# Kernel optimization log

Hardware: AMD Instinct MI355X
Metric: run time of the kernel (lower is better)

The kernel has to match this reference:

```python
import jax, jax.numpy as jnp
import numpy as np

IN_FEATURES = 1024
OUT_FEATURES = 1024
GRID_SIZE = 5
SPLINE_ORDER = 3
GRID_RANGE = (-1.0, 1.0)


def make_grid():
    h = (GRID_RANGE[1] - GRID_RANGE[0]) / GRID_SIZE
    knots = jnp.arange(-SPLINE_ORDER, GRID_SIZE + SPLINE_ORDER + 1, dtype=jnp.float32) * h + GRID_RANGE[0]
    return jnp.broadcast_to(knots, (IN_FEATURES, knots.shape[0]))  # (in, 12)


def b_splines(x, knots, p):
    # x: (B, in); knots: (in, nk). Cox-de Boor recursion, degree p.
    xs = x[:, :, None]                                   # (B, in, 1)
    bases = ((xs >= knots[None, :, :-1]) & (xs < knots[None, :, 1:])).astype(x.dtype)
    for k in range(1, p + 1):
        den1 = knots[:, k:-1] - knots[:, :-(k + 1)]
        den1 = jnp.where(den1 == 0, jnp.float32(1e-8), den1)
        den2 = knots[:, k + 1:] - knots[:, 1:-k]
        den2 = jnp.where(den2 == 0, jnp.float32(1e-8), den2)
        term1 = (xs - knots[None, :, :-(k + 1)]) / den1[None] * bases[:, :, :-1]
        term2 = (knots[None, :, k + 1:] - xs) / den2[None] * bases[:, :, 1:]
        bases = term1 + term2
    return bases  # (B, in, grid_size + p)


def setup_inputs() -> dict:
    key = jax.random.key(0)
    k1, k2, k3, k4 = jax.random.split(key, 4)
    K = GRID_SIZE + SPLINE_ORDER
    x = jax.random.normal(k1, (4096, IN_FEATURES), dtype=jnp.float32)
    base_weight = jax.random.normal(k2, (OUT_FEATURES, IN_FEATURES), dtype=jnp.float32) * (1.0 / np.sqrt(IN_FEATURES))
    spline_weight = jax.random.normal(k3, (OUT_FEATURES, IN_FEATURES, K), dtype=jnp.float32) * 0.02
    spline_scaler = jax.random.normal(k4, (OUT_FEATURES, IN_FEATURES), dtype=jnp.float32) * (1.0 / np.sqrt(IN_FEATURES))
    grid = make_grid()
    return {"x": x, "base_weight": base_weight, "spline_weight": spline_weight,
            "spline_scaler": spline_scaler, "grid": grid}


def reference(x, base_weight, spline_weight, spline_scaler, grid):
    base_out = jax.nn.silu(x) @ base_weight.T                      # (B, out)
    bases = b_splines(x, grid, SPLINE_ORDER)                       # (B, in, K)
    scaled_sw = spline_weight * spline_scaler[:, :, None]          # (out, in, K)
    spline_out = jnp.einsum('bik,oik->bo', bases, scaled_sw)       # (B, out)
    return base_out + spline_out
```

## Files before the change

kernel.cpp:

```cpp
#include <hip/hip_runtime.h>
#include <hip/hip_bf16.h>
#include <cstdint>
#include <cstddef>

#define AS1 __attribute__((address_space(1)))
#define AS3 __attribute__((address_space(3)))

typedef __bf16 bf16;
typedef __bf16 bf16x8 __attribute__((ext_vector_type(8)));
typedef float f32x4 __attribute__((ext_vector_type(4)));

static constexpr int M_ROWS = 4096;
static constexpr int N_COLS = 1024;
static constexpr int IN_F   = 1024;
static constexpr int K2     = IN_F * 9;
static constexpr int BK     = 32;
static constexpr int KT_CNT = K2 / BK;

static constexpr int GBK = 64;
static constexpr int GKT = K2 / GBK;


__device__ __forceinline__ void bases8(float x, float w8[8]) {
  float mf = x * 2.5f + 5.5f;
  int   m  = (int)floorf(mf);
  float u  = mf - (float)m;
  float u2 = u * u, u3 = u2 * u;
  float omu = 1.0f - u;
  const float s = 1.0f / 6.0f;
  float p0 = u3 * s;
  float p1 = (-3.f*u3 + 3.f*u2 + 3.f*u + 1.f) * s;
  float p2 = (3.f*u3 - 6.f*u2 + 4.f) * s;
  float p3 = omu * omu * omu * s;
  bool in = (m >= 0) && (m < 11);
#pragma unroll
  for (int j = 0; j < 8; ++j) {
    float v = 0.0f;
    v = (j == m)     ? p0 : v;
    v = (j == m - 1) ? p1 : v;
    v = (j == m - 2) ? p2 : v;
    v = (j == m - 3) ? p3 : v;
    w8[j] = in ? v : 0.0f;
  }
}

__device__ __forceinline__ void expand_body(const float* __restrict__ x,
                                            bf16* __restrict__ A, int gid, int r0) {
  int b = gid >> 10;
  int i = gid & 1023;
  float xv = x[(size_t)r0 * IN_F + (size_t)gid];
  A[(size_t)b * K2 + i] = (bf16)(xv / (1.0f + __expf(-xv)));
  float w8[8];
  bases8(xv, w8);
  bf16x8 outv;
#pragma unroll
  for (int j = 0; j < 8; ++j) outv[j] = (bf16)w8[j];
  *(bf16x8*)(A + (size_t)b * K2 + IN_F + (size_t)i * 8) = outv;
}

__device__ __forceinline__ void makebt_body(const float* __restrict__ bw,
                                            const float* __restrict__ sw,
                                            const float* __restrict__ sc,
                                            bf16* __restrict__ BT, int gid) {
  int o = gid >> 10;
  int i = gid & 1023;
  BT[(size_t)o * K2 + i] = (bf16)bw[gid];
  float scale = sc[gid];
  const float4* swp = (const float4*)(sw + (size_t)gid * 8);
  float4 a = swp[0], b4 = swp[1];
  float wv[8] = {a.x, a.y, a.z, a.w, b4.x, b4.y, b4.z, b4.w};
  bf16x8 r;
#pragma unroll
  for (int j = 0; j < 8; ++j) r[j] = (bf16)(wv[j] * scale);
  *(bf16x8*)(BT + (size_t)o * K2 + IN_F + (size_t)i * 8) = r;
}

__global__ void prep(const float* __restrict__ x, const float* __restrict__ bw,
                     const float* __restrict__ sw, const float* __restrict__ sc,
                     bf16* __restrict__ A, bf16* __restrict__ BT) {
  int bid = blockIdx.x;
  if (bid < (M_ROWS * IN_F) / 256) {
    expand_body(x, A, bid * 256 + threadIdx.x, 0);
  } else {
    makebt_body(bw, sw, sc, BT, (bid - (M_ROWS * IN_F) / 256) * 256 + threadIdx.x);
  }
}

__global__ void expand_a(const float* __restrict__ x, bf16* __restrict__ A, int r0) {
  expand_body(x, A, blockIdx.x * blockDim.x + threadIdx.x, r0);
}
__global__ void make_bt(const float* __restrict__ bw, const float* __restrict__ sw,
                        const float* __restrict__ sc, bf16* __restrict__ BT) {
  makebt_body(bw, sw, sc, BT, blockIdx.x * blockDim.x + threadIdx.x);
}

__global__ __launch_bounds__(512, 2) void gemm256_8p(
    const bf16* __restrict__ A, const bf16* __restrict__ BT,
    float* __restrict__ P, int kt_seg) {
  __shared__ bf16 As[2][256 * GBK];
  __shared__ bf16 Bs[2][256 * GBK];

  const int tid  = threadIdx.x;
  const int lane = tid & 63;
  const int w    = tid >> 6;

  const int b     = blockIdx.x;
  const int mtile = b & 15;
  const int np    = (b >> 4) & 3;
  const int seg   = b >> 6;
  const int row0  = mtile * 256;
  const int col0  = np * 256;
  const int kt0   = seg * kt_seg;
  float* __restrict__ dst = P + (size_t)seg * M_ROWS * N_COLS;

  const int srow = lane >> 3;
  const int sch  = ((lane & 7) ^ srow) * 8;

  const int r  = lane & 15;
  const int q  = lane >> 4;
  const int wm = (w >> 2) * 128;
  const int wn = (w & 3) * 64;
  const int kc0 = ((0 + q) ^ (r & 7)) * 8;
  const int kc1 = ((4 + q) ^ (r & 7)) * 8;

  const bf16* aB = A  + (size_t)row0 * K2;
  const bf16* bB = BT + (size_t)col0 * K2;

  f32x4 acc[8][4];
#pragma unroll
  for (int mt = 0; mt < 8; ++mt)
#pragma unroll
    for (int nt = 0; nt < 4; ++nt)
      acc[mt][nt] = f32x4{0.f, 0.f, 0.f, 0.f};

  auto stageA = [&](int sbuf, int h, int kt) {
#pragma unroll
    for (int t8 = 0; t8 < 2; ++t8) {
      const int rg = h * 128 + w * 16 + t8 * 8;
      const bf16* ga = aB + (size_t)(rg + srow) * K2 + kt * GBK + sch;
      __builtin_amdgcn_global_load_lds((const AS1 void*)ga,
                                       (AS3 void*)&As[sbuf][rg * GBK], 16, 0, 0);
    }
  };
  auto stageB = [&](int sbuf, int h, int kt) {
#pragma unroll
    for (int t8 = 0; t8 < 2; ++t8) {
      const int rg = h * 128 + w * 16 + t8 * 8;
      const bf16* gb = bB + (size_t)(rg + srow) * K2 + kt * GBK + sch;
      __builtin_amdgcn_global_load_lds((const AS1 void*)gb,
                                       (AS3 void*)&Bs[sbuf][rg * GBK], 16, 0, 0);
    }
  };

  stageA(0, 0, kt0); stageA(0, 1, kt0);
  stageB(0, 0, kt0); stageB(0, 1, kt0);
  if (kt_seg > 1) stageA(1, 0, kt0 + 1);
  if (kt_seg > 1) asm volatile("s_waitcnt vmcnt(2)" ::: "memory");
  else            asm volatile("s_waitcnt vmcnt(0)" ::: "memory");
  __builtin_amdgcn_s_barrier();

  bf16x8 af[4][2], bfr[4][2];

  for (int t = 0; t < kt_seg; ++t) {
    const int buf = t & 1, nbuf = buf ^ 1;
    const bf16* as = As[buf];
    const bf16* bs = Bs[buf];
    const bool sN = (t + 1 < kt_seg);

#pragma unroll
    for (int j = 0; j < 4; ++j) {
      const bf16* ar = &as[(wm + j * 16 + r) * GBK];
      af[j][0] = *(const bf16x8*)&ar[kc0];
      af[j][1] = *(const bf16x8*)&ar[kc1];
    }
#pragma unroll
    for (int j = 0; j < 2; ++j) {
      const bf16* br = &bs[(wn + j * 16 + r) * GBK];
      bfr[j][0] = *(const bf16x8*)&br[kc0];
      bfr[j][1] = *(const bf16x8*)&br[kc1];
    }
    if (sN) stageA(nbuf, 1, kt0 + t + 1);
    asm volatile("s_waitcnt lgkmcnt(8)" ::: "memory");
    __builtin_amdgcn_s_barrier();
    asm volatile("s_waitcnt lgkmcnt(0)" ::: "memory");
    __builtin_amdgcn_sched_barrier(0);
    __builtin_amdgcn_s_setprio(1);
#pragma unroll
    for (int j = 0; j < 4; ++j)
#pragma unroll
      for (int n = 0; n < 2; ++n) {
        acc[j][n] = __builtin_amdgcn_mfma_f32_16x16x32_bf16(af[j][0], bfr[n][0], acc[j][n], 0, 0, 0);
        acc[j][n] = __builtin_amdgcn_mfma_f32_16x16x32_bf16(af[j][1], bfr[n][1], acc[j][n], 0, 0, 0);
      }
    __builtin_amdgcn_s_setprio(0);
    __builtin_amdgcn_s_barrier();

#pragma unroll
    for (int j = 0; j < 2; ++j) {
      const bf16* br = &bs[(wn + (2 + j) * 16 + r) * GBK];
      bfr[2 + j][0] = *(const bf16x8*)&br[kc0];
      bfr[2 + j][1] = *(const bf16x8*)&br[kc1];
    }
    if (sN) stageB(nbuf, 0, kt0 + t + 1);
    __builtin_amdgcn_s_barrier();
    asm volatile("s_waitcnt lgkmcnt(0)" ::: "memory");
    __builtin_amdgcn_sched_barrier(0);
    __builtin_amdgcn_s_setprio(1);
#pragma unroll
    for (int j = 0; j < 4; ++j)
#pragma unroll
      for (int n = 0; n < 2; ++n) {
        acc[j][2 + n] = __builtin_amdgcn_mfma_f32_16x16x32_bf16(af[j][0], bfr[2 + n][0], acc[j][2 + n], 0, 0, 0);
        acc[j][2 + n] = __builtin_amdgcn_mfma_f32_16x16x32_bf16(af[j][1], bfr[2 + n][1], acc[j][2 + n], 0, 0, 0);
      }
    __builtin_amdgcn_s_setprio(0);
    __builtin_amdgcn_s_barrier();

#pragma unroll
    for (int j = 0; j < 4; ++j) {
      const bf16* ar = &as[(wm + (4 + j) * 16 + r) * GBK];
      af[j][0] = *(const bf16x8*)&ar[kc0];
      af[j][1] = *(const bf16x8*)&ar[kc1];
    }
    if (sN) stageB(nbuf, 1, kt0 + t + 1);
    __builtin_amdgcn_s_barrier();
    asm volatile("s_waitcnt lgkmcnt(0)" ::: "memory");
    __builtin_amdgcn_sched_barrier(0);
    __builtin_amdgcn_s_setprio(1);
#pragma unroll
    for (int j = 0; j < 4; ++j)
#pragma unroll
      for (int n = 0; n < 2; ++n) {
        acc[4 + j][n] = __builtin_amdgcn_mfma_f32_16x16x32_bf16(af[j][0], bfr[n][0], acc[4 + j][n], 0, 0, 0);
        acc[4 + j][n] = __builtin_amdgcn_mfma_f32_16x16x32_bf16(af[j][1], bfr[n][1], acc[4 + j][n], 0, 0, 0);
      }
    __builtin_amdgcn_s_setprio(0);
    __builtin_amdgcn_s_barrier();

    if (t + 2 < kt_seg) stageA(buf, 0, kt0 + t + 2);
    if (sN) {
      if (t + 2 < kt_seg) asm volatile("s_waitcnt vmcnt(2)" ::: "memory");
      else                asm volatile("s_waitcnt vmcnt(0)" ::: "memory");
    }
    __builtin_amdgcn_s_barrier();
    __builtin_amdgcn_s_setprio(1);
#pragma unroll
    for (int j = 0; j < 4; ++j)
#pragma unroll
      for (int n = 0; n < 2; ++n) {
        acc[4 + j][2 + n] = __builtin_amdgcn_mfma_f32_16x16x32_bf16(af[j][0], bfr[2 + n][0], acc[4 + j][2 + n], 0, 0, 0);
        acc[4 + j][2 + n] = __builtin_amdgcn_mfma_f32_16x16x32_bf16(af[j][1], bfr[2 + n][1], acc[4 + j][2 + n], 0, 0, 0);
      }
    __builtin_amdgcn_s_setprio(0);
    __builtin_amdgcn_s_barrier();
  }

#pragma unroll
  for (int mt = 0; mt < 8; ++mt)
#pragma unroll
    for (int nt = 0; nt < 4; ++nt)
#pragma unroll
      for (int k = 0; k < 4; ++k) {
        int row = row0 + wm + mt * 16 + q * 4 + k;
        int col = col0 + wn + nt * 16 + r;
        dst[(size_t)row * N_COLS + col] = acc[mt][nt][k];
      }
}

__global__ __launch_bounds__(256, 2) void gemm_fused(
    const bf16* __restrict__ A, const bf16* __restrict__ BT,
    float* __restrict__ d0, float* __restrict__ d1,
    int r0, int mt_cnt, int kt_seg) {
  __shared__ bf16 As[2][128 * GBK];
  __shared__ bf16 Bs[2][128 * GBK];

  const int tid  = threadIdx.x;
  const int lane = tid & 63;
  const int w    = tid >> 6;

  const int bps = mt_cnt * 8;
  int b   = blockIdx.x;
  const int seg = b / bps;
  b -= seg * bps;
  const int row0 = (b % mt_cnt) * 128;
  const int col0 = (b / mt_cnt) * 128;
  float* __restrict__ dst = seg ? d1 : d0;
  const int kt0 = seg * kt_seg;

  const int srow = lane >> 3;
  const int sch  = ((lane & 7) ^ srow) * 8;
  const int r  = lane & 15;
  const int q  = lane >> 4;
  const int wm = (w >> 1) * 64;
  const int wn = (w & 1) * 64;
  const int kc0 = ((0 + q) ^ (r & 7)) * 8;
  const int kc1 = ((4 + q) ^ (r & 7)) * 8;

  const bf16* aB = A  + (size_t)row0 * K2;
  const bf16* bB = BT + (size_t)col0 * K2;

  f32x4 acc[4][4];
#pragma unroll
  for (int mt = 0; mt < 4; ++mt)
#pragma unroll
    for (int nt = 0; nt < 4; ++nt)
      acc[mt][nt] = f32x4{0.f, 0.f, 0.f, 0.f};

  auto stage = [&](int sbuf, int kt) {
#pragma unroll
    for (int t = 0; t < 4; ++t) {
      const int rg = w * 32 + t * 8;
      const bf16* ga = aB + (size_t)(rg + srow) * K2 + kt * GBK + sch;
      __builtin_amdgcn_global_load_lds((const AS1 void*)ga,
                                       (AS3 void*)&As[sbuf][rg * GBK], 16, 0, 0);
      const bf16* gb = bB + (size_t)(rg + srow) * K2 + kt * GBK + sch;
      __builtin_amdgcn_global_load_lds((const AS1 void*)gb,
                                       (AS3 void*)&Bs[sbuf][rg * GBK], 16, 0, 0);
    }
  };

  stage(0, kt0);
  int buf = 0;
  for (int i = 0; i < kt_seg; ++i) {
    if (i + 1 < kt_seg) {
      stage(buf ^ 1, kt0 + i + 1);
      asm volatile("s_waitcnt vmcnt(8)" ::: "memory");
    } else {
      asm volatile("s_waitcnt vmcnt(0)" ::: "memory");
    }
    __builtin_amdgcn_s_barrier();
    __builtin_amdgcn_sched_barrier(0);

    const bf16* as = As[buf];
    const bf16* bs = Bs[buf];

#pragma unroll
    for (int kk = 0; kk < 2; ++kk) {
      const int kc = kk ? kc1 : kc0;
      bf16x8 af[4], bfr[4];
#pragma unroll
      for (int mt = 0; mt < 4; ++mt)
        af[mt] = *(const bf16x8*)&as[(wm + mt * 16 + r) * GBK + kc];
#pragma unroll
      for (int nt = 0; nt < 4; ++nt)
        bfr[nt] = *(const bf16x8*)&bs[(wn + nt * 16 + r) * GBK + kc];
#pragma unroll
      for (int mt = 0; mt < 4; ++mt)
#pragma unroll
        for (int nt = 0; nt < 4; ++nt)
          acc[mt][nt] = __builtin_amdgcn_mfma_f32_16x16x32_bf16(
              af[mt], bfr[nt], acc[mt][nt], 0, 0, 0);
    }
    __builtin_amdgcn_s_barrier();
    buf ^= 1;
  }

#pragma unroll
  for (int mt = 0; mt < 4; ++mt)
#pragma unroll
    for (int nt = 0; nt < 4; ++nt)
#pragma unroll
      for (int k = 0; k < 4; ++k) {
        int row = r0 + row0 + wm + mt * 16 + q * 4 + k;
        int col = col0 + wn + nt * 16 + r;
        dst[(size_t)row * N_COLS + col] = acc[mt][nt][k];
      }
}

__global__ void reduce_addN(const float* __restrict__ P,
                            float* __restrict__ out, int segs) {
  size_t i = (size_t)blockIdx.x * blockDim.x + threadIdx.x;
  const f32x4* p = (const f32x4*)P;
  const size_t plane = (size_t)M_ROWS * N_COLS / 4;
  f32x4 a = p[i];
  for (int s = 1; s < segs; ++s) a += p[(size_t)s * plane + i];
  ((f32x4*)out)[i] = a;
}

__global__ __launch_bounds__(256) void kan_fused_fallback(
    const float* __restrict__ x, const float* __restrict__ bw,
    const float* __restrict__ sw, const float* __restrict__ sc,
    float* __restrict__ out) {
  __shared__ bf16 As[64 * BK];
  __shared__ bf16 Bs[128 * BK];
  const int tid  = threadIdx.x;
  const int lane = tid & 63;
  const int w    = tid >> 6;
  const int col0 = blockIdx.x * 128;
  const int row0 = blockIdx.y * 64;
  const int srow = tid >> 2, sq = tid & 3;
  const int r = lane & 15, q = lane >> 4, wn = w * 32;

  f32x4 acc[4][2];
#pragma unroll
  for (int mt = 0; mt < 4; ++mt)
#pragma unroll
    for (int nt = 0; nt < 2; ++nt) acc[mt][nt] = f32x4{0,0,0,0};

  for (int kt = 0; kt < KT_CNT; ++kt) {
    if (kt < 32) {
      const int cc = sq * 8;
      const float4* xp = (const float4*)(x + (size_t)(row0+srow)*IN_F + kt*BK + cc);
      float4 a = xp[0], b4 = xp[1];
      float xv[8] = {a.x,a.y,a.z,a.w,b4.x,b4.y,b4.z,b4.w};
      bf16x8 av;
#pragma unroll
      for (int j = 0; j < 8; ++j) av[j] = (bf16)(xv[j] / (1.0f + __expf(-xv[j])));
      *(bf16x8*)&As[srow * BK + cc] = av;
#pragma unroll
      for (int h = 0; h < 2; ++h) {
        const float4* bp = (const float4*)(bw + (size_t)(col0+h*64+srow)*IN_F + kt*BK + cc);
        float4 c0 = bp[0], c1 = bp[1];
        float bv[8] = {c0.x,c0.y,c0.z,c0.w,c1.x,c1.y,c1.z,c1.w};
        bf16x8 bb;
#pragma unroll
        for (int j = 0; j < 8; ++j) bb[j] = (bf16)bv[j];
        *(bf16x8*)&Bs[(h*64+srow)*BK + cc] = bb;
      }
    } else {
      const int i = (kt - 32) * 4 + sq;
      float xv = x[(size_t)(row0+srow)*IN_F + i];
      float w8[8]; bases8(xv, w8);
      bf16x8 av;
#pragma unroll
      for (int j = 0; j < 8; ++j) av[j] = (bf16)w8[j];
      *(bf16x8*)&As[srow * BK + sq * 8] = av;
#pragma unroll
      for (int h = 0; h < 2; ++h) {
        const int o = col0 + h*64 + srow;
        float s1 = sc[(size_t)o*IN_F + i];
        const float4* sp = (const float4*)(sw + ((size_t)o*IN_F + i)*8);
        float4 c0 = sp[0], c1 = sp[1];
        float wv[8] = {c0.x,c0.y,c0.z,c0.w,c1.x,c1.y,c1.z,c1.w};
        bf16x8 bb;
#pragma unroll
        for (int j = 0; j < 8; ++j) bb[j] = (bf16)(wv[j]*s1);
        *(bf16x8*)&Bs[(h*64+srow)*BK + sq*8] = bb;
      }
    }
    __syncthreads();
    bf16x8 af[4], bfr[2];
#pragma unroll
    for (int mt = 0; mt < 4; ++mt)
      af[mt] = *(const bf16x8*)&As[(mt*16+r)*BK + q*8];
#pragma unroll
    for (int nt = 0; nt < 2; ++nt)
      bfr[nt] = *(const bf16x8*)&Bs[(wn+nt*16+r)*BK + q*8];
#pragma unroll
    for (int mt = 0; mt < 4; ++mt)
#pragma unroll
      for (int nt = 0; nt < 2; ++nt)
        acc[mt][nt] = __builtin_amdgcn_mfma_f32_16x16x32_bf16(af[mt], bfr[nt], acc[mt][nt], 0,0,0);
    __syncthreads();
  }
#pragma unroll
  for (int mt = 0; mt < 4; ++mt)
#pragma unroll
    for (int nt = 0; nt < 2; ++nt)
#pragma unroll
      for (int k = 0; k < 4; ++k)
        out[(size_t)(row0+mt*16+q*4+k)*N_COLS + col0+wn+nt*16+r] = acc[mt][nt][k];
}

extern "C" void kernel_launch(void* const* d_in, const int* in_sizes, int n_in,
                              void* d_out, int out_size, void* d_ws, size_t ws_size,
                              hipStream_t stream) {
  const float* x    = (const float*)d_in[0];
  const float* bw   = (const float*)d_in[1];
  const float* sw   = (const float*)d_in[2];
  const float* sc   = (const float*)d_in[3];
  float* out = (float*)d_out;

  const size_t BT_BYTES  = (size_t)N_COLS * K2 * sizeof(bf16);
  const size_t ROW_BYTES = (size_t)K2 * sizeof(bf16);
  const size_t A_BYTES   = (size_t)M_ROWS * ROW_BYTES;
  const size_t OUT_BYTES = (size_t)M_ROWS * N_COLS * sizeof(float);

  int S = 0;
  for (int c = 4; c >= 2; --c)
    if (GKT % c == 0 && BT_BYTES + A_BYTES + (size_t)c * OUT_BYTES <= ws_size) {
      S = c; break;
    }

  if (S >= 2) {
    bf16*  BT    = (bf16*)d_ws;
    bf16*  Aslab = BT + (size_t)N_COLS * K2;
    float* P     = (float*)((char*)d_ws + BT_BYTES + A_BYTES);
    prep<<<(M_ROWS * IN_F) / 256 + (N_COLS * IN_F) / 256, 256, 0, stream>>>(
        x, bw, sw, sc, Aslab, BT);
    gemm256_8p<<<S * 64, 512, 0, stream>>>(Aslab, BT, P, GKT / S);
    reduce_addN<<<(M_ROWS * N_COLS) / (4 * 256), 256, 0, stream>>>(P, out, S);
  } else {
    int SL = 0;
    for (int cand = 4096; cand >= 128; cand >>= 1)
      if (BT_BYTES + (size_t)cand * ROW_BYTES <= ws_size) { SL = cand; break; }
    if (SL) {
      bf16* BT    = (bf16*)d_ws;
      bf16* Aslab = BT + (size_t)N_COLS * K2;
      make_bt<<<(N_COLS * IN_F) / 256, 256, 0, stream>>>(bw, sw, sc, BT);
      for (int r0 = 0; r0 < M_ROWS; r0 += SL) {
        expand_a<<<(SL * IN_F) / 256, 256, 0, stream>>>(x, Aslab, r0);
        gemm_fused<<<(SL / 128) * (N_COLS / 128), 256, 0, stream>>>(
            Aslab, BT, out, out, r0, SL / 128, GKT);
      }
    } else {
      kan_fused_fallback<<<dim3(N_COLS / 128, M_ROWS / 64), 256, 0, stream>>>(
          x, bw, sw, sc, out);
    }
  }
  (void)in_sizes; (void)n_in; (void)out_size;
}
```

Baseline: 201.2 us.

## Software-pipeline LDS fragment reads across K-tiles with reordered MFMA quadrants

Restructures the main GEMM loop so each quadrant's LDS fragment reads are issued one MFMA phase ahead. The first A and B fragments of the next K-tile are prefetched during the last MFMA phase of the current tile, and the loop is unrolled by two to ping-pong the B fragment registers. This cuts the number of barriers per tile and hides LDS latency behind MFMA work, at the cost of more live registers. The host now requires an even number of K-tiles per split.

```diff
diff --git a/kernel.cpp b/kernel.cpp
--- a/kernel.cpp
+++ b/kernel.cpp
@@ -94,7 +94,7 @@
   makebt_body(bw, sw, sc, BT, blockIdx.x * blockDim.x + threadIdx.x);
 }
 
-__global__ __launch_bounds__(512, 2) void gemm256_8p(
+__global__ __launch_bounds__(512, 2) void gemm256_pl(
     const bf16* __restrict__ A, const bf16* __restrict__ BT,
     float* __restrict__ P, int kt_seg) {
   __shared__ bf16 As[2][256 * GBK];
@@ -133,6 +133,8 @@
     for (int nt = 0; nt < 4; ++nt)
       acc[mt][nt] = f32x4{0.f, 0.f, 0.f, 0.f};
 
+  bf16x8 af03[4][2], af47[4][2], bf23[2][2], bf01A[2][2], bf01B[2][2];
+
   auto stageA = [&](int sbuf, int h, int kt) {
 #pragma unroll
     for (int t8 = 0; t8 < 2; ++t8) {
@@ -152,107 +154,125 @@
     }
   };
 
-  stageA(0, 0, kt0); stageA(0, 1, kt0);
-  stageB(0, 0, kt0); stageB(0, 1, kt0);
-  if (kt_seg > 1) stageA(1, 0, kt0 + 1);
-  if (kt_seg > 1) asm volatile("s_waitcnt vmcnt(2)" ::: "memory");
-  else            asm volatile("s_waitcnt vmcnt(0)" ::: "memory");
-  __builtin_amdgcn_s_barrier();
-
-  bf16x8 af[4][2], bfr[4][2];
-
-  for (int t = 0; t < kt_seg; ++t) {
-    const int buf = t & 1, nbuf = buf ^ 1;
-    const bf16* as = As[buf];
-    const bf16* bs = Bs[buf];
+  auto readA03 = [&](const bf16* src) {
+#pragma unroll
+    for (int j = 0; j < 4; ++j) {
+      const bf16* ar = &src[(wm + j * 16 + r) * GBK];
+      af03[j][0] = *(const bf16x8*)&ar[kc0];
+      af03[j][1] = *(const bf16x8*)&ar[kc1];
+    }
+  };
+  auto readA47 = [&](const bf16* src) {
+#pragma unroll
+    for (int j = 0; j < 4; ++j) {
+      const bf16* ar = &src[(wm + (4 + j) * 16 + r) * GBK];
+      af47[j][0] = *(const bf16x8*)&ar[kc0];
+      af47[j][1] = *(const bf16x8*)&ar[kc1];
+    }
+  };
+  auto readB23 = [&](const bf16* src) {
+#pragma unroll
+    for (int j = 0; j < 2; ++j) {
+      const bf16* br = &src[(wn + (2 + j) * 16 + r) * GBK];
+      bf23[j][0] = *(const bf16x8*)&br[kc0];
+      bf23[j][1] = *(const bf16x8*)&br[kc1];
+    }
+  };
+  auto readB01 = [&](bf16x8 (&dstf)[2][2], const bf16* src) {
+#pragma unroll
+    for (int j = 0; j < 2; ++j) {
+      const bf16* br = &src[(wn + j * 16 + r) * GBK];
+      dstf[j][0] = *(const bf16x8*)&br[kc0];
+      dstf[j][1] = *(const bf16x8*)&br[kc1];
+    }
+  };
+
+  auto tile_body = [&](int t, int nb, const bf16* as, const bf16* bs,
+                       const bf16* nas, const bf16* nbs,
+                       bf16x8 (&bfc)[2][2], bf16x8 (&bfn)[2][2]) {
     const bool sN = (t + 1 < kt_seg);
 
-#pragma unroll
-    for (int j = 0; j < 4; ++j) {
-      const bf16* ar = &as[(wm + j * 16 + r) * GBK];
-      af[j][0] = *(const bf16x8*)&ar[kc0];
-      af[j][1] = *(const bf16x8*)&ar[kc1];
-    }
-#pragma unroll
-    for (int j = 0; j < 2; ++j) {
-      const bf16* br = &bs[(wn + j * 16 + r) * GBK];
-      bfr[j][0] = *(const bf16x8*)&br[kc0];
-      bfr[j][1] = *(const bf16x8*)&br[kc1];
-    }
-    if (sN) stageA(nbuf, 1, kt0 + t + 1);
+    readB23(bs);
+    if (sN) stageA(nb, 1, kt0 + t + 1);
+    asm volatile("s_waitcnt lgkmcnt(4)" ::: "memory");
+    __builtin_amdgcn_sched_barrier(0);
+    __builtin_amdgcn_s_barrier();
+    __builtin_amdgcn_s_setprio(1);
+#pragma unroll
+    for (int j = 0; j < 4; ++j)
+#pragma unroll
+      for (int n = 0; n < 2; ++n) {
+        acc[j][n] = __builtin_amdgcn_mfma_f32_16x16x32_bf16(af03[j][0], bfc[n][0], acc[j][n], 0, 0, 0);
+        acc[j][n] = __builtin_amdgcn_mfma_f32_16x16x32_bf16(af03[j][1], bfc[n][1], acc[j][n], 0, 0, 0);
+      }
+    __builtin_amdgcn_s_setprio(0);
+
+    readA47(as);
+    if (sN) stageB(nb, 0, kt0 + t + 1);
     asm volatile("s_waitcnt lgkmcnt(8)" ::: "memory");
+    __builtin_amdgcn_sched_barrier(0);
     __builtin_amdgcn_s_barrier();
+    __builtin_amdgcn_s_setprio(1);
+#pragma unroll
+    for (int j = 0; j < 4; ++j)
+#pragma unroll
+      for (int n = 0; n < 2; ++n) {
+        acc[j][2 + n] = __builtin_amdgcn_mfma_f32_16x16x32_bf16(af03[j][0], bf23[n][0], acc[j][2 + n], 0, 0, 0);
+        acc[j][2 + n] = __builtin_amdgcn_mfma_f32_16x16x32_bf16(af03[j][1], bf23[n][1], acc[j][2 + n], 0, 0, 0);
+      }
+    __builtin_amdgcn_s_setprio(0);
+
+    if (sN) stageB(nb, 1, kt0 + t + 1);
     asm volatile("s_waitcnt lgkmcnt(0)" ::: "memory");
     __builtin_amdgcn_sched_barrier(0);
+    __builtin_amdgcn_s_barrier();
     __builtin_amdgcn_s_setprio(1);
 #pragma unroll
     for (int j = 0; j < 4; ++j)
 #pragma unroll
       for (int n = 0; n < 2; ++n) {
-        acc[j][n] = __builtin_amdgcn_mfma_f32_16x16x32_bf16(af[j][0], bfr[n][0], acc[j][n], 0, 0, 0);
-        acc[j][n] = __builtin_amdgcn_mfma_f32_16x16x32_bf16(af[j][1], bfr[n][1], acc[j][n], 0, 0, 0);
+        acc[4 + j][2 + n] = __builtin_amdgcn_mfma_f32_16x16x32_bf16(af47[j][0], bf23[n][0], acc[4 + j][2 + n], 0, 0, 0);
+        acc[4 + j][2 + n] = __builtin_amdgcn_mfma_f32_16x16x32_bf16(af47[j][1], bf23[n][1], acc[4 + j][2 + n], 0, 0, 0);
       }
     __builtin_amdgcn_s_setprio(0);
-    __builtin_amdgcn_s_barrier();
-
-#pragma unroll
-    for (int j = 0; j < 2; ++j) {
-      const bf16* br = &bs[(wn + (2 + j) * 16 + r) * GBK];
-      bfr[2 + j][0] = *(const bf16x8*)&br[kc0];
-      bfr[2 + j][1] = *(const bf16x8*)&br[kc1];
-    }
-    if (sN) stageB(nbuf, 0, kt0 + t + 1);
-    __builtin_amdgcn_s_barrier();
-    asm volatile("s_waitcnt lgkmcnt(0)" ::: "memory");
-    __builtin_amdgcn_sched_barrier(0);
-    __builtin_amdgcn_s_setprio(1);
-#pragma unroll
-    for (int j = 0; j < 4; ++j)
-#pragma unroll
-      for (int n = 0; n < 2; ++n) {
-        acc[j][2 + n] = __builtin_amdgcn_mfma_f32_16x16x32_bf16(af[j][0], bfr[2 + n][0], acc[j][2 + n], 0, 0, 0);
-        acc[j][2 + n] = __builtin_amdgcn_mfma_f32_16x16x32_bf16(af[j][1], bfr[2 + n][1], acc[j][2 + n], 0, 0, 0);
-      }
-    __builtin_amdgcn_s_setprio(0);
-    __builtin_amdgcn_s_barrier();
-
-#pragma unroll
-    for (int j = 0; j < 4; ++j) {
-      const bf16* ar = &as[(wm + (4 + j) * 16 + r) * GBK];
-      af[j][0] = *(const bf16x8*)&ar[kc0];
-      af[j][1] = *(const bf16x8*)&ar[kc1];
-    }
-    if (sN) stageB(nbuf, 1, kt0 + t + 1);
-    __builtin_amdgcn_s_barrier();
-    asm volatile("s_waitcnt lgkmcnt(0)" ::: "memory");
-    __builtin_amdgcn_sched_barrier(0);
-    __builtin_amdgcn_s_setprio(1);
-#pragma unroll
-    for (int j = 0; j < 4; ++j)
-#pragma unroll
-      for (int n = 0; n < 2; ++n) {
-        acc[4 + j][n] = __builtin_amdgcn_mfma_f32_16x16x32_bf16(af[j][0], bfr[n][0], acc[4 + j][n], 0, 0, 0);
-        acc[4 + j][n] = __builtin_amdgcn_mfma_f32_16x16x32_bf16(af[j][1], bfr[n][1], acc[4 + j][n], 0, 0, 0);
-      }
-    __builtin_amdgcn_s_setprio(0);
-    __builtin_amdgcn_s_barrier();
-
-    if (t + 2 < kt_seg) stageA(buf, 0, kt0 + t + 2);
+
+    if (t + 2 < kt_seg) stageA(nb ^ 1, 0, kt0 + t + 2);
     if (sN) {
       if (t + 2 < kt_seg) asm volatile("s_waitcnt vmcnt(2)" ::: "memory");
       else                asm volatile("s_waitcnt vmcnt(0)" ::: "memory");
     }
     __builtin_amdgcn_s_barrier();
+    if (sN) {
+      readA03(nas);
+      readB01(bfn, nbs);
+    }
+    __builtin_amdgcn_sched_barrier(0);
     __builtin_amdgcn_s_setprio(1);
 #pragma unroll
     for (int j = 0; j < 4; ++j)
 #pragma unroll
       for (int n = 0; n < 2; ++n) {
-        acc[4 + j][2 + n] = __builtin_amdgcn_mfma_f32_16x16x32_bf16(af[j][0], bfr[2 + n][0], acc[4 + j][2 + n], 0, 0, 0);
-        acc[4 + j][2 + n] = __builtin_amdgcn_mfma_f32_16x16x32_bf16(af[j][1], bfr[2 + n][1], acc[4 + j][2 + n], 0, 0, 0);
+        acc[4 + j][n] = __builtin_amdgcn_mfma_f32_16x16x32_bf16(af47[j][0], bfc[n][0], acc[4 + j][n], 0, 0, 0);
+        acc[4 + j][n] = __builtin_amdgcn_mfma_f32_16x16x32_bf16(af47[j][1], bfc[n][1], acc[4 + j][n], 0, 0, 0);
       }
     __builtin_amdgcn_s_setprio(0);
-    __builtin_amdgcn_s_barrier();
+  };
+
+  stageA(0, 0, kt0); stageA(0, 1, kt0);
+  stageB(0, 0, kt0); stageB(0, 1, kt0);
+  if (kt_seg > 1) {
+    stageA(1, 0, kt0 + 1);
+    asm volatile("s_waitcnt vmcnt(2)" ::: "memory");
+  } else {
+    asm volatile("s_waitcnt vmcnt(0)" ::: "memory");
+  }
+  __builtin_amdgcn_s_barrier();
+  readA03(As[0]);
+  readB01(bf01A, Bs[0]);
+
+  for (int tt = 0; tt < kt_seg; tt += 2) {
+    tile_body(tt,     1, As[0], Bs[0], As[1], Bs[1], bf01A, bf01B);
+    tile_body(tt + 1, 0, As[1], Bs[1], As[0], Bs[0], bf01B, bf01A);
   }
 
 #pragma unroll
@@ -478,7 +498,8 @@
 
   int S = 0;
   for (int c = 4; c >= 2; --c)
-    if (GKT % c == 0 && BT_BYTES + A_BYTES + (size_t)c * OUT_BYTES <= ws_size) {
+    if (GKT % c == 0 && ((GKT / c) % 2 == 0) &&
+        BT_BYTES + A_BYTES + (size_t)c * OUT_BYTES <= ws_size) {
       S = c; break;
     }
 
@@ -488,7 +509,7 @@
     float* P     = (float*)((char*)d_ws + BT_BYTES + A_BYTES);
     prep<<<(M_ROWS * IN_F) / 256 + (N_COLS * IN_F) / 256, 256, 0, stream>>>(
         x, bw, sw, sc, Aslab, BT);
-    gemm256_8p<<<S * 64, 512, 0, stream>>>(Aslab, BT, P, GKT / S);
+    gemm256_pl<<<S * 64, 512, 0, stream>>>(Aslab, BT, P, GKT / S);
     reduce_addN<<<(M_ROWS * N_COLS) / (4 * 256), 256, 0, stream>>>(P, out, S);
   } else {
     int SL = 0;
```

After: 266.0 us. +32.2%, slower.

## Collapse four-phase GEMM main loop into two phases with fewer barriers

Applied to the files above, without the earlier changes.

Restructures the 256x256 MFMA main loop so each k-step loads all B fragments up front and issues all next-tile global-to-LDS stages at once. The four barrier-separated compute phases become two, removing most workgroup barriers per iteration and reusing B fragments across the two A halves. The cost is more live B registers (bf01/bf23 held together) and clustered global loads, which may hurt latency hiding or occupancy. reduce_addN is moved earlier in the file with no functional change.

```diff
diff --git a/kernel.cpp b/kernel.cpp
--- a/kernel.cpp
+++ b/kernel.cpp
@@ -159,7 +159,7 @@
   else            asm volatile("s_waitcnt vmcnt(0)" ::: "memory");
   __builtin_amdgcn_s_barrier();
 
-  bf16x8 af[4][2], bfr[4][2];
+  bf16x8 af[4][2], bf01[2][2], bf23[2][2];
 
   for (int t = 0; t < kt_seg; ++t) {
     const int buf = t & 1, nbuf = buf ^ 1;
@@ -176,12 +176,33 @@
 #pragma unroll
     for (int j = 0; j < 2; ++j) {
       const bf16* br = &bs[(wn + j * 16 + r) * GBK];
-      bfr[j][0] = *(const bf16x8*)&br[kc0];
-      bfr[j][1] = *(const bf16x8*)&br[kc1];
-    }
-    if (sN) stageA(nbuf, 1, kt0 + t + 1);
-    asm volatile("s_waitcnt lgkmcnt(8)" ::: "memory");
-    __builtin_amdgcn_s_barrier();
+      bf01[j][0] = *(const bf16x8*)&br[kc0];
+      bf01[j][1] = *(const bf16x8*)&br[kc1];
+    }
+#pragma unroll
+    for (int j = 0; j < 2; ++j) {
+      const bf16* br = &bs[(wn + (2 + j) * 16 + r) * GBK];
+      bf23[j][0] = *(const bf16x8*)&br[kc0];
+      bf23[j][1] = *(const bf16x8*)&br[kc1];
+    }
+    if (sN) {
+      stageA(nbuf, 1, kt0 + t + 1);
+      stageB(nbuf, 0, kt0 + t + 1);
+      stageB(nbuf, 1, kt0 + t + 1);
+    }
+
+    asm volatile("s_waitcnt lgkmcnt(4)" ::: "memory");
+    __builtin_amdgcn_sched_barrier(0);
+    __builtin_amdgcn_s_setprio(1);
+#pragma unroll
+    for (int j = 0; j < 4; ++j)
+#pragma unroll
+      for (int n = 0; n < 2; ++n) {
+        acc[j][n] = __builtin_amdgcn_mfma_f32_16x16x32_bf16(af[j][0], bf01[n][0], acc[j][n], 0, 0, 0);
+        acc[j][n] = __builtin_amdgcn_mfma_f32_16x16x32_bf16(af[j][1], bf01[n][1], acc[j][n], 0, 0, 0);
+      }
+    __builtin_amdgcn_s_setprio(0);
+
     asm volatile("s_waitcnt lgkmcnt(0)" ::: "memory");
     __builtin_amdgcn_sched_barrier(0);
     __builtin_amdgcn_s_setprio(1);
@@ -189,32 +210,10 @@
     for (int j = 0; j < 4; ++j)
 #pragma unroll
       for (int n = 0; n < 2; ++n) {
-        acc[j][n] = __builtin_amdgcn_mfma_f32_16x16x32_bf16(af[j][0], bfr[n][0], acc[j][n], 0, 0, 0);
-        acc[j][n] = __builtin_amdgcn_mfma_f32_16x16x32_bf16(af[j][1], bfr[n][1], acc[j][n], 0, 0, 0);
+        acc[j][2 + n] = __builtin_amdgcn_mfma_f32_16x16x32_bf16(af[j][0], bf23[n][0], acc[j][2 + n], 0, 0, 0);
+        acc[j][2 + n] = __builtin_amdgcn_mfma_f32_16x16x32_bf16(af[j][1], bf23[n][1], acc[j][2 + n], 0, 0, 0);
       }
     __builtin_amdgcn_s_setprio(0);
-    __builtin_amdgcn_s_barrier();
-
-#pragma unroll
-    for (int j = 0; j < 2; ++j) {
-      const bf16* br = &bs[(wn + (2 + j) * 16 + r) * GBK];
-      bfr[2 + j][0] = *(const bf16x8*)&br[kc0];
-      bfr[2 + j][1] = *(const bf16x8*)&br[kc1];
-    }
-    if (sN) stageB(nbuf, 0, kt0 + t + 1);
-    __builtin_amdgcn_s_barrier();
-    asm volatile("s_waitcnt lgkmcnt(0)" ::: "memory");
-    __builtin_amdgcn_sched_barrier(0);
-    __builtin_amdgcn_s_setprio(1);
-#pragma unroll
-    for (int j = 0; j < 4; ++j)
-#pragma unroll
-      for (int n = 0; n < 2; ++n) {
-        acc[j][2 + n] = __builtin_amdgcn_mfma_f32_16x16x32_bf16(af[j][0], bfr[2 + n][0], acc[j][2 + n], 0, 0, 0);
-        acc[j][2 + n] = __builtin_amdgcn_mfma_f32_16x16x32_bf16(af[j][1], bfr[2 + n][1], acc[j][2 + n], 0, 0, 0);
-      }
-    __builtin_amdgcn_s_setprio(0);
-    __builtin_amdgcn_s_barrier();
 
 #pragma unroll
     for (int j = 0; j < 4; ++j) {
@@ -222,8 +221,6 @@
       af[j][0] = *(const bf16x8*)&ar[kc0];
       af[j][1] = *(const bf16x8*)&ar[kc1];
     }
-    if (sN) stageB(nbuf, 1, kt0 + t + 1);
-    __builtin_amdgcn_s_barrier();
     asm volatile("s_waitcnt lgkmcnt(0)" ::: "memory");
     __builtin_amdgcn_sched_barrier(0);
     __builtin_amdgcn_s_setprio(1);
@@ -231,28 +228,25 @@
     for (int j = 0; j < 4; ++j)
 #pragma unroll
       for (int n = 0; n < 2; ++n) {
-        acc[4 + j][n] = __builtin_amdgcn_mfma_f32_16x16x32_bf16(af[j][0], bfr[n][0], acc[4 + j][n], 0, 0, 0);
-        acc[4 + j][n] = __builtin_amdgcn_mfma_f32_16x16x32_bf16(af[j][1], bfr[n][1], acc[4 + j][n], 0, 0, 0);
+        acc[4 + j][2 + n] = __builtin_amdgcn_mfma_f32_16x16x32_bf16(af[j][0], bf23[n][0], acc[4 + j][2 + n], 0, 0, 0);
+        acc[4 + j][2 + n] = __builtin_amdgcn_mfma_f32_16x16x32_bf16(af[j][1], bf23[n][1], acc[4 + j][2 + n], 0, 0, 0);
+      }
+#pragma unroll
+    for (int j = 0; j < 4; ++j)
+#pragma unroll
+      for (int n = 0; n < 2; ++n) {
+        acc[4 + j][n] = __builtin_amdgcn_mfma_f32_16x16x32_bf16(af[j][0], bf01[n][0], acc[4 + j][n], 0, 0, 0);
+        acc[4 + j][n] = __builtin_amdgcn_mfma_f32_16x16x32_bf16(af[j][1], bf01[n][1], acc[4 + j][n], 0, 0, 0);
       }
     __builtin_amdgcn_s_setprio(0);
+
     __builtin_amdgcn_s_barrier();
-
     if (t + 2 < kt_seg) stageA(buf, 0, kt0 + t + 2);
     if (sN) {
       if (t + 2 < kt_seg) asm volatile("s_waitcnt vmcnt(2)" ::: "memory");
       else                asm volatile("s_waitcnt vmcnt(0)" ::: "memory");
-    }
-    __builtin_amdgcn_s_barrier();
-    __builtin_amdgcn_s_setprio(1);
-#pragma unroll
-    for (int j = 0; j < 4; ++j)
-#pragma unroll
-      for (int n = 0; n < 2; ++n) {
-        acc[4 + j][2 + n] = __builtin_amdgcn_mfma_f32_16x16x32_bf16(af[j][0], bfr[2 + n][0], acc[4 + j][2 + n], 0, 0, 0);
-        acc[4 + j][2 + n] = __builtin_amdgcn_mfma_f32_16x16x32_bf16(af[j][1], bfr[2 + n][1], acc[4 + j][2 + n], 0, 0, 0);
-      }
-    __builtin_amdgcn_s_setprio(0);
-    __builtin_amdgcn_s_barrier();
+      __builtin_amdgcn_s_barrier();
+    }
   }
 
 #pragma unroll
@@ -265,6 +259,16 @@
         int col = col0 + wn + nt * 16 + r;
         dst[(size_t)row * N_COLS + col] = acc[mt][nt][k];
       }
+}
+
+__global__ void reduce_addN(const float* __restrict__ P,
+                            float* __restrict__ out, int segs) {
+  size_t i = (size_t)blockIdx.x * blockDim.x + threadIdx.x;
+  const f32x4* p = (const f32x4*)P;
+  const size_t plane = (size_t)M_ROWS * N_COLS / 4;
+  f32x4 a = p[i];
+  for (int s = 1; s < segs; ++s) a += p[(size_t)s * plane + i];
+  ((f32x4*)out)[i] = a;
 }
 
 __global__ __launch_bounds__(256, 2) void gemm_fused(
@@ -365,16 +369,6 @@
         int col = col0 + wn + nt * 16 + r;
         dst[(size_t)row * N_COLS + col] = acc[mt][nt][k];
       }
-}
-
-__global__ void reduce_addN(const float* __restrict__ P,
-                            float* __restrict__ out, int segs) {
-  size_t i = (size_t)blockIdx.x * blockDim.x + threadIdx.x;
-  const f32x4* p = (const f32x4*)P;
-  const size_t plane = (size_t)M_ROWS * N_COLS / 4;
-  f32x4 a = p[i];
-  for (int s = 1; s < segs; ++s) a += p[(size_t)s * plane + i];
-  ((f32x4*)out)[i] = a;
 }
 
 __global__ __launch_bounds__(256) void kan_fused_fallback(
```

New measurement: 199.1 us. No clear change (-1.1%).
